# Optimization experiments

Measured on AMD Instinct MI355X. Metric: run time of the kernel, lower is better.

Reference implementation:

```python
import jax, jax.numpy as jnp
import numpy as np

EPS = 1e-3  # Q = eps * I(5) in the original module

def setup_inputs() -> dict:
    key = jax.random.key(0)
    k1, k2, k3 = jax.random.split(key, 3)
    B, n = 4194304, 5
    x = jax.random.normal(k1, (B, n), dtype=jnp.float32)
    # fc1 = nn.Linear(n, n): weight [n, n], bias [n]
    W = jax.random.normal(k2, (n, n), dtype=jnp.float32) * (1.0 / np.sqrt(n))
    b_fc = jax.random.normal(k3, (n,), dtype=jnp.float32) * 0.1
    return {"x": x, "W": W, "b_fc": b_fc}

def reference(x, W, b_fc):
    # h = fc1(x)  (the QP inequality RHS per sample)
    h = x @ W.T + b_fc  # [B, 5]
    # Per-sample QP: min_z 0.5*eps*||z||^2 + 1^T z  s.t.  -z <= h  (G = -I)
    # Separable closed form (exact solution cvxopt converges to):
    #   unconstrained minimizer z_i = -1/eps; constraint z_i >= -h_i
    #   => z_i = max(-h_i, -1/eps)
    z = jnp.maximum(-h, -1.0 / EPS)  # [B, 5] primal solutions
    return z
```

## Files before the change

kernel.cpp:

```cpp
#include <hip/hip_runtime.h>


#define BLOCK 256
#define WAVES_PER_BLOCK 4
#define F4_PER_TILE 320
#define TILES_PER_WAVE 4

typedef float vf4 __attribute__((ext_vector_type(4)));

__global__ __launch_bounds__(BLOCK) void qpnet_kernel(
    const float* __restrict__ x,
    const float* __restrict__ W,
    const float* __restrict__ bfc,
    float* __restrict__ out,
    int total_f4)
{
    __shared__ __align__(16) float lds[BLOCK * 20];

    float w[5][5];
    float bias[5];
#pragma unroll
    for (int j = 0; j < 5; ++j) {
        bias[j] = bfc[j];
#pragma unroll
        for (int i = 0; i < 5; ++i) w[j][i] = W[j * 5 + i];
    }

    const int wave = threadIdx.x >> 6;
    const int lane = threadIdx.x & 63;
    float* __restrict__ wlds = &lds[wave * (64 * 20)];

    const int wave_id = blockIdx.x * WAVES_PER_BLOCK + wave;
    const int tb = wave_id * (F4_PER_TILE * TILES_PER_WAVE);
    if (tb >= total_f4) return;

    const vf4* __restrict__ xin  = reinterpret_cast<const vf4*>(x);
    vf4* __restrict__       zout = reinterpret_cast<vf4*>(out);

    vf4 r[5];
#pragma unroll
    for (int k = 0; k < 5; ++k) r[k] = xin[tb + k * 64 + lane];

#pragma unroll
    for (int t = 0; t < TILES_PER_WAVE; ++t) {
        const int cur = tb + t * F4_PER_TILE;

#pragma unroll
        for (int k = 0; k < 5; ++k)
            *reinterpret_cast<vf4*>(&wlds[(k * 64 + lane) * 4]) = r[k];

        vf4 rn[5];
        if (t + 1 < TILES_PER_WAVE) {
            const int nxt = cur + F4_PER_TILE;
#pragma unroll
            for (int k = 0; k < 5; ++k) rn[k] = xin[nxt + k * 64 + lane];
        }
        __builtin_amdgcn_sched_barrier(0);

        asm volatile("s_waitcnt lgkmcnt(0)" ::: "memory");

        float v[20];
#pragma unroll
        for (int p = 0; p < 5; ++p)
            *reinterpret_cast<vf4*>(&v[4 * p]) =
                *reinterpret_cast<const vf4*>(&wlds[lane * 20 + 4 * p]);

#pragma unroll
        for (int k = 0; k < 4; ++k) {
            float t0 = bias[0], t1 = bias[1], t2 = bias[2], t3 = bias[3], t4 = bias[4];
#pragma unroll
            for (int i = 0; i < 5; ++i) {
                const float xv = v[k * 5 + i];
                t0 = fmaf(xv, w[0][i], t0);
                t1 = fmaf(xv, w[1][i], t1);
                t2 = fmaf(xv, w[2][i], t2);
                t3 = fmaf(xv, w[3][i], t3);
                t4 = fmaf(xv, w[4][i], t4);
            }
            v[k * 5 + 0] = fmaxf(-t0, -1000.0f);
            v[k * 5 + 1] = fmaxf(-t1, -1000.0f);
            v[k * 5 + 2] = fmaxf(-t2, -1000.0f);
            v[k * 5 + 3] = fmaxf(-t3, -1000.0f);
            v[k * 5 + 4] = fmaxf(-t4, -1000.0f);
        }

#pragma unroll
        for (int p = 0; p < 5; ++p)
            *reinterpret_cast<vf4*>(&wlds[lane * 20 + 4 * p]) =
                *reinterpret_cast<const vf4*>(&v[4 * p]);
        asm volatile("s_waitcnt lgkmcnt(0)" ::: "memory");

#pragma unroll
        for (int k = 0; k < 5; ++k)
            zout[cur + k * 64 + lane] =
                *reinterpret_cast<const vf4*>(&wlds[(k * 64 + lane) * 4]);

        if (t + 1 < TILES_PER_WAVE) {
#pragma unroll
            for (int k = 0; k < 5; ++k) r[k] = rn[k];
        }
    }
}

extern "C" void kernel_launch(void* const* d_in, const int* in_sizes, int n_in,
                              void* d_out, int out_size, void* d_ws, size_t ws_size,
                              hipStream_t stream) {
    const float* x   = (const float*)d_in[0];
    const float* W   = (const float*)d_in[1];
    const float* bfc = (const float*)d_in[2];
    float* out = (float*)d_out;

    int total_f4 = in_sizes[0] / 4;
    int f4_per_wave = F4_PER_TILE * TILES_PER_WAVE;
    int n_waves  = (total_f4 + f4_per_wave - 1) / f4_per_wave;
    int grid     = (n_waves + WAVES_PER_BLOCK - 1) / WAVES_PER_BLOCK;

    qpnet_kernel<<<grid, BLOCK, 0, stream>>>(x, W, bfc, out, total_f4);
}
```

Measured before the change: 152.8 us.

## Load input tiles directly into double-buffered LDS via global_load_lds

Input tiles now go straight from global memory into a per-wave double-buffered LDS region using global_load_lds, instead of passing through VGPRs and ds_write. Explicit vmcnt waits sequence the prefetch of the next tile against compute on the current one. This removes the register staging and LDS write traffic for the input. The cost is twice the LDS per block, which can lower occupancy, and correctness now depends on hand-tuned vmcnt counts that also count the global stores.

```diff
diff --git a/kernel.cpp b/kernel.cpp
--- a/kernel.cpp
+++ b/kernel.cpp
@@ -5,8 +5,12 @@
 #define WAVES_PER_BLOCK 4
 #define F4_PER_TILE 320
 #define TILES_PER_WAVE 4
+#define TILE_FLOATS 1280
 
 typedef float vf4 __attribute__((ext_vector_type(4)));
+
+typedef const __attribute__((address_space(1))) void gvoid_t;
+typedef __attribute__((address_space(3))) void svoid_t;
 
 __global__ __launch_bounds__(BLOCK) void qpnet_kernel(
     const float* __restrict__ x,
@@ -15,7 +19,7 @@
     float* __restrict__ out,
     int total_f4)
 {
-    __shared__ __align__(16) float lds[BLOCK * 20];
+    __shared__ __align__(16) float lds[WAVES_PER_BLOCK * 2 * TILE_FLOATS];
 
     float w[5][5];
     float bias[5];
@@ -28,7 +32,7 @@
 
     const int wave = threadIdx.x >> 6;
     const int lane = threadIdx.x & 63;
-    float* __restrict__ wlds = &lds[wave * (64 * 20)];
+    float* const wbuf = &lds[wave * (2 * TILE_FLOATS)];
 
     const int wave_id = blockIdx.x * WAVES_PER_BLOCK + wave;
     const int tb = wave_id * (F4_PER_TILE * TILES_PER_WAVE);
@@ -37,33 +41,43 @@
     const vf4* __restrict__ xin  = reinterpret_cast<const vf4*>(x);
     vf4* __restrict__       zout = reinterpret_cast<vf4*>(out);
 
-    vf4 r[5];
 #pragma unroll
-    for (int k = 0; k < 5; ++k) r[k] = xin[tb + k * 64 + lane];
+    for (int k = 0; k < 5; ++k) {
+        __builtin_amdgcn_global_load_lds(
+            (gvoid_t*)(const void*)&xin[tb + k * 64 + lane],
+            (svoid_t*)(void*)&wbuf[k * 256], 16, 0, 0);
+    }
 
 #pragma unroll
     for (int t = 0; t < TILES_PER_WAVE; ++t) {
         const int cur = tb + t * F4_PER_TILE;
+        float* const cbuf = wbuf + (t & 1) * TILE_FLOATS;
 
-#pragma unroll
-        for (int k = 0; k < 5; ++k)
-            *reinterpret_cast<vf4*>(&wlds[(k * 64 + lane) * 4]) = r[k];
-
-        vf4 rn[5];
         if (t + 1 < TILES_PER_WAVE) {
+            float* const nbuf = wbuf + ((t + 1) & 1) * TILE_FLOATS;
             const int nxt = cur + F4_PER_TILE;
 #pragma unroll
-            for (int k = 0; k < 5; ++k) rn[k] = xin[nxt + k * 64 + lane];
+            for (int k = 0; k < 5; ++k) {
+                __builtin_amdgcn_global_load_lds(
+                    (gvoid_t*)(const void*)&xin[nxt + k * 64 + lane],
+                    (svoid_t*)(void*)&nbuf[k * 256], 16, 0, 0);
+            }
+        }
+
+        if (t == 0) {
+            asm volatile("s_waitcnt vmcnt(5)" ::: "memory");
+        } else if (t + 1 < TILES_PER_WAVE) {
+            asm volatile("s_waitcnt vmcnt(10)" ::: "memory");
+        } else {
+            asm volatile("s_waitcnt vmcnt(5)" ::: "memory");
         }
         __builtin_amdgcn_sched_barrier(0);
-
-        asm volatile("s_waitcnt lgkmcnt(0)" ::: "memory");
 
         float v[20];
 #pragma unroll
         for (int p = 0; p < 5; ++p)
             *reinterpret_cast<vf4*>(&v[4 * p]) =
-                *reinterpret_cast<const vf4*>(&wlds[lane * 20 + 4 * p]);
+                *reinterpret_cast<const vf4*>(&cbuf[lane * 20 + 4 * p]);
 
 #pragma unroll
         for (int k = 0; k < 4; ++k) {
@@ -86,19 +100,14 @@
 
 #pragma unroll
         for (int p = 0; p < 5; ++p)
-            *reinterpret_cast<vf4*>(&wlds[lane * 20 + 4 * p]) =
+            *reinterpret_cast<vf4*>(&cbuf[lane * 20 + 4 * p]) =
                 *reinterpret_cast<const vf4*>(&v[4 * p]);
         asm volatile("s_waitcnt lgkmcnt(0)" ::: "memory");
 
 #pragma unroll
         for (int k = 0; k < 5; ++k)
             zout[cur + k * 64 + lane] =
-                *reinterpret_cast<const vf4*>(&wlds[(k * 64 + lane) * 4]);
-
-        if (t + 1 < TILES_PER_WAVE) {
-#pragma unroll
-            for (int k = 0; k < 5; ++k) r[k] = rn[k];
-        }
+                *reinterpret_cast<const vf4*>(&cbuf[(k * 64 + lane) * 4]);
     }
 }
 
```

Measured after the change: 151.4 us. No clear change (-0.9%).
